# Kernel tuning notes

Measured on AMD Instinct MI355X. Metric: run time of the kernel, lower is better.

The kernel has to match this reference:

```python
import jax, jax.numpy as jnp
import numpy as np

D_MODEL = 1024
N_HEADS = 16
D_HEAD = D_MODEL // N_HEADS  # 64
NUM_MEM_KV = 4
SCALE = D_HEAD ** -0.5


def setup_inputs() -> dict:
    key = jax.random.key(0)
    k1, k2, k3, k4 = jax.random.split(key, 4)
    x = jax.random.normal(k1, (4, 4096, D_MODEL), dtype=jnp.float32)
    mask = jax.random.randint(k2, (4, 4096), 0, 2).astype(jnp.int32)
    w_qkv = jax.random.normal(k3, (3 * D_MODEL, D_MODEL), dtype=jnp.float32) * 0.02
    mem_kv = jax.random.normal(k4, (2, N_HEADS, NUM_MEM_KV, D_HEAD), dtype=jnp.float32)
    return {"x": x, "w_qkv": w_qkv, "mem_kv": mem_kv, "mask": mask}


def reference(x, w_qkv, mem_kv, mask):
    b, l, _ = x.shape
    # qkv projection: nn.Linear applies x @ W^T; reshape matches torch view(..., h, d_head, 3)
    qkv = jnp.einsum('bld,ed->ble', x, w_qkv).reshape(b, l, N_HEADS, D_HEAD, 3)
    qkv = jnp.moveaxis(qkv, 2, 1)  # (b, h, l, d_head, 3)
    q, k, v = qkv[..., 0], qkv[..., 1], qkv[..., 2]

    m = mask.astype(x.dtype)[:, None, :, None]  # (b, 1, l, 1) per prepare_mask
    k = jnp.where(m == 0, -jnp.inf, k * m)

    # prepend learned memory kv along the sequence axis
    mk = jnp.broadcast_to(mem_kv[0], (b, N_HEADS, NUM_MEM_KV, D_HEAD))
    mv = jnp.broadcast_to(mem_kv[1], (b, N_HEADS, NUM_MEM_KV, D_HEAD))
    k = jnp.concatenate([mk, k], axis=-2)  # (b, h, m+l, d_head)
    v = jnp.concatenate([mv, v], axis=-2)

    q = jax.nn.softmax(q * SCALE, axis=-1)   # softmax over feature dim
    k = jax.nn.softmax(k, axis=-2)           # softmax over sequence dim; -inf rows -> 0 weight

    context = jnp.einsum('bhnd,bhne->bhde', k, v)   # (b, h, d_head, d_head)
    out = jnp.einsum('bhld,bhde->bhle', q, context)  # (b, h, l, d_head)
    out = out * m
    out = jnp.moveaxis(out, 1, 2).reshape(b, l, N_HEADS * D_HEAD)
    return out
```

## Files before the change

kernel.cpp:

```cpp
#include <hip/hip_runtime.h>

typedef _Float16 h8 __attribute__((ext_vector_type(8)));
typedef _Float16 h4 __attribute__((ext_vector_type(4)));
typedef float f4 __attribute__((ext_vector_type(4)));

typedef __attribute__((address_space(1))) const void GV;
typedef __attribute__((address_space(3))) void SV;

__device__ __forceinline__ void async16(const void* g, void* s) {
  __builtin_amdgcn_global_load_lds((GV*)g, (SV*)s, 16, 0, 0);
}


#define XC 2097152
#define WC 393216
#define ZC 4194304

__global__ __launch_bounds__(1024) void compact(const int4* __restrict__ mask4,
                                                int* __restrict__ cnt,
                                                int* __restrict__ idx) {
  const int b = blockIdx.x;
  const int t = threadIdx.x;
  const int lane = t & 63, w = t >> 6;

  const int4 m4 = mask4[b * 1024 + t];
  int m[4] = {m4.x, m4.y, m4.z, m4.w};
  const int c = (m[0] != 0) + (m[1] != 0) + (m[2] != 0) + (m[3] != 0);

  int inc = c;
#pragma unroll
  for (int off = 1; off < 64; off <<= 1) {
    const int v = __shfl_up(inc, off);
    if (lane >= off) inc += v;
  }
  __shared__ int wtot[16];
  if (lane == 63) wtot[w] = inc;
  __syncthreads();
  int prev = 0;
#pragma unroll
  for (int i = 0; i < 16; ++i)
    if (i < w) prev += wtot[i];
  const int excl = prev + inc - c;

  if (t == 1023) cnt[b] = excl + c;

  int* const ib = idx + b * 4096;
  int p = excl;
  int q = t * 4 - excl;
#pragma unroll
  for (int r = 0; r < 4; ++r) {
    const int row = t * 4 + r;
    if (m[r]) ib[p++] = row;
    else      ib[4095 - q++] = row;
  }
}

__global__ __launch_bounds__(256) void cvt_f16(const float4* __restrict__ x,
                                               const float4* __restrict__ w,
                                               const int* __restrict__ mask,
                                               h8* __restrict__ xh,
                                               h8* __restrict__ wh,
                                               float4* __restrict__ out) {
  int t = blockIdx.x * 256 + threadIdx.x;
  if (t < XC) {
    const int row = t >> 7, c7 = t & 127;
    const int dst = (row << 7) | (c7 & 120) | ((c7 & 7) ^ (row & 7));
    float4 a = x[t * 2], b = x[t * 2 + 1];
    h8 o = {(_Float16)a.x, (_Float16)a.y, (_Float16)a.z, (_Float16)a.w,
            (_Float16)b.x, (_Float16)b.y, (_Float16)b.z, (_Float16)b.w};
    xh[dst] = o;
  } else if (t < XC + WC) {
    const int u = t - XC;
    const int rp = u >> 7, c7 = u & 127;
    int sr;
    if (rp < 2048) {
      int h = rp >> 7, c = rp & 127;
      sr = h * 192 + ((c < 64) ? (c * 3 + 1) : ((c - 64) * 3 + 2));
    } else {
      int q = rp - 2048;
      sr = (q >> 6) * 192 + (q & 63) * 3;
    }
    const int dst = (rp << 7) | (c7 & 120) | ((c7 & 7) ^ (rp & 7));
    float4 a = w[sr * 256 + c7 * 2], b = w[sr * 256 + c7 * 2 + 1];
    h8 o = {(_Float16)a.x, (_Float16)a.y, (_Float16)a.z, (_Float16)a.w,
            (_Float16)b.x, (_Float16)b.y, (_Float16)b.z, (_Float16)b.w};
    wh[dst] = o;
  } else {
    const int u = t - (XC + WC);
    const int row = u >> 8, c = u & 255;
    if (!mask[row]) {
      const float4 z4 = {0.f, 0.f, 0.f, 0.f};
      out[(size_t)row * 256 + c] = z4;
    }
  }
}

__global__ __launch_bounds__(256, 3) void kv_gemm(const _Float16* __restrict__ A,
                                                  const _Float16* __restrict__ W,
                                                  const int* __restrict__ cnt,
                                                  const int* __restrict__ idx,
                                                  float* __restrict__ part) {
  const int my = blockIdx.y;
  const int b = my >> 5, lc = my & 31;
  const int cb = cnt[b];
  if (lc * 128 >= cb) return;

  __shared__ _Float16 smem[128 * 128];
  _Float16* const As = smem;
  _Float16* const Bs = smem + 8192;
  const int tid = threadIdx.x;
  const int lane = tid & 63, wid = tid >> 6;
  const int wm = wid & 1, wn = wid >> 1;
  const int l15 = lane & 15, quad = lane >> 4;
  const int n0 = blockIdx.x * 128;

  int rsrc[4], x7[4];
#pragma unroll
  for (int it = 0; it < 4; ++it) {
    const int s = it * 32 + (tid >> 3);
    const int ri = idx[b * 4096 + lc * 128 + s];
    rsrc[it] = b * 4096 + ri;
    x7[it] = (s & 7) ^ (ri & 7);
  }
  const int cg = tid & 7;

  const f4 z = {0.f, 0.f, 0.f, 0.f};
  f4 acc[4][4];
#pragma unroll
  for (int i = 0; i < 4; ++i)
#pragma unroll
    for (int j = 0; j < 4; ++j) acc[i][j] = z;

  const int swz = l15 & 7;

  for (int kt = 0; kt < 16; ++kt) {
    const int k0 = kt * 64;
#pragma unroll
    for (int it = 0; it < 4; ++it) {
      const int idxl = it * 256 + tid;
      const int brow = idxl >> 3;
      async16(A + ((size_t)rsrc[it] * 1024 + k0 + (cg ^ x7[it]) * 8), As + idxl * 8);
      async16(W + ((size_t)(n0 + brow) * 1024 + k0 + cg * 8), Bs + idxl * 8);
    }
    __syncthreads();
#pragma unroll
    for (int ks = 0; ks < 2; ++ks) {
      const int pc = ((ks << 2) | quad) ^ swz;
      h8 af[4], bf[4];
#pragma unroll
      for (int i = 0; i < 4; ++i)
        af[i] = *(const h8*)&As[(wm * 64 + i * 16 + l15) * 64 + pc * 8];
#pragma unroll
      for (int j = 0; j < 4; ++j)
        bf[j] = *(const h8*)&Bs[(wn * 64 + j * 16 + l15) * 64 + pc * 8];
#pragma unroll
      for (int i = 0; i < 4; ++i)
#pragma unroll
        for (int j = 0; j < 4; ++j)
          acc[i][j] = __builtin_amdgcn_mfma_f32_16x16x32_f16(af[i], bf[j], acc[i][j], 0, 0, 0);
    }
    __syncthreads();
  }

  const int h = n0 >> 7;
  const int bh = b * 16 + h;
  const int jbase = lc * 128;
#pragma unroll
  for (int i = 0; i < 4; ++i) {
    const int nb = wm * 64 + i * 16 + quad * 4;
#pragma unroll
    for (int j = 0; j < 4; ++j) {
      const int c = wn * 64 + j * 16 + l15;
      h4 o;
      if (wn == 0) {
#pragma unroll
        for (int r = 0; r < 4; ++r)
          o[r] = (_Float16)((jbase + nb + r < cb) ? __expf(acc[i][j][r]) : 0.f);
      } else {
#pragma unroll
        for (int r = 0; r < 4; ++r) o[r] = (_Float16)acc[i][j][r];
      }
      *(h4*)&smem[c * 128 + (nb ^ (l15 * 8))] = o;
    }
  }
  __syncthreads();
  f4 cacc[5];
#pragma unroll
  for (int i = 0; i < 5; ++i) cacc[i] = z;
  h8 bones;
  {
    const _Float16 o1 = (l15 == 0) ? (_Float16)1.f : (_Float16)0.f;
#pragma unroll
    for (int j = 0; j < 8; ++j) bones[j] = o1;
  }
  const int ds = wid * 16;
#pragma unroll
  for (int ks = 0; ks < 4; ++ks) {
    const int nb2 = (ks * 32 + quad * 8) ^ (l15 * 8);
    h8 a = *(const h8*)&smem[(ds + l15) * 128 + nb2];
#pragma unroll
    for (int et = 0; et < 4; ++et) {
      h8 bv = *(const h8*)&smem[(64 + et * 16 + l15) * 128 + nb2];
      cacc[et] = __builtin_amdgcn_mfma_f32_16x16x32_f16(a, bv, cacc[et], 0, 0, 0);
    }
    cacc[4] = __builtin_amdgcn_mfma_f32_16x16x32_f16(a, bones, cacc[4], 0, 0, 0);
  }
  const size_t pb = ((size_t)bh * 32 + lc) * 4160;
  const int dw = ds + quad * 4;
#pragma unroll
  for (int et = 0; et < 4; ++et)
#pragma unroll
    for (int r = 0; r < 4; ++r)
      part[pb + (size_t)(dw + r) * 64 + et * 16 + l15] = cacc[et][r];
  if (l15 == 0) {
#pragma unroll
    for (int r = 0; r < 4; ++r) part[pb + 4096 + dw + r] = cacc[4][r];
  }
}

__global__ __launch_bounds__(256) void reduce_ctx(const float* __restrict__ part,
                                                  const float* __restrict__ memkv,
                                                  const int* __restrict__ cnt,
                                                  _Float16* __restrict__ ctxt) {
  const int bh = blockIdx.x;
  const int dsl = blockIdx.y;
  const int h = bh & 15;
  const int tid = threadIdx.x;
  const int dl = tid >> 6, e = tid & 63;
  const int d = dsl * 4 + dl;
  const size_t pb = (size_t)bh * 32 * 4160;
  const int nch = (cnt[bh >> 4] + 127) >> 7;

  float den = 0.f;
  for (int c = 0; c < nch; ++c) den += part[pb + (size_t)c * 4160 + 4096 + d];
  float s = 0.f;
  for (int c = 0; c < nch; ++c) s += part[pb + (size_t)c * 4160 + (size_t)d * 64 + e];
#pragma unroll
  for (int j = 0; j < 4; ++j) {
    const float ek = __expf(memkv[(h * 4 + j) * 64 + d]);
    den += ek;
    s += ek * memkv[4096 + (h * 4 + j) * 64 + e];
  }
  ctxt[(size_t)bh * 4096 + (size_t)e * 64 + d] = (_Float16)(s / den);
}

__global__ __launch_bounds__(256, 3) void qpv(const _Float16* __restrict__ A,
                                              const _Float16* __restrict__ W,
                                              const _Float16* __restrict__ ctxt,
                                              const int* __restrict__ cnt,
                                              const int* __restrict__ idx,
                                              float* __restrict__ out) {
  const int my = blockIdx.y;
  const int b = my >> 5, lc = my & 31;
  const int cb = cnt[b];
  if (lc * 128 >= cb) return;

  __shared__ _Float16 smem[128 * 128];
  _Float16* const As = smem;
  _Float16* const Bs = smem + 8192;
  const int tid = threadIdx.x;
  const int lane = tid & 63, wid = tid >> 6;
  const int wm = wid & 1, wn = wid >> 1;
  const int l15 = lane & 15, quad = lane >> 4;
  const int n0 = blockIdx.x * 128;

  int rsrc[4], x7[4];
#pragma unroll
  for (int it = 0; it < 4; ++it) {
    const int s = it * 32 + (tid >> 3);
    const int ri = idx[b * 4096 + lc * 128 + s];
    rsrc[it] = b * 4096 + ri;
    x7[it] = (s & 7) ^ (ri & 7);
  }
  const int cg = tid & 7;

  const f4 z = {0.f, 0.f, 0.f, 0.f};
  f4 acc[4][4];
#pragma unroll
  for (int i = 0; i < 4; ++i)
#pragma unroll
    for (int j = 0; j < 4; ++j) acc[i][j] = z;

  const int swz = l15 & 7;

  for (int kt = 0; kt < 16; ++kt) {
    const int k0 = kt * 64;
#pragma unroll
    for (int it = 0; it < 4; ++it) {
      const int idxl = it * 256 + tid;
      const int brow = idxl >> 3;
      async16(A + ((size_t)rsrc[it] * 1024 + k0 + (cg ^ x7[it]) * 8), As + idxl * 8);
      async16(W + ((size_t)(2048 + n0 + brow) * 1024 + k0 + cg * 8), Bs + idxl * 8);
    }
    __syncthreads();
#pragma unroll
    for (int ks = 0; ks < 2; ++ks) {
      const int pc = ((ks << 2) | quad) ^ swz;
      h8 af[4], bf[4];
#pragma unroll
      for (int i = 0; i < 4; ++i)
        af[i] = *(const h8*)&As[(wm * 64 + i * 16 + l15) * 64 + pc * 8];
#pragma unroll
      for (int j = 0; j < 4; ++j)
        bf[j] = *(const h8*)&Bs[(wn * 64 + j * 16 + l15) * 64 + pc * 8];
#pragma unroll
      for (int i = 0; i < 4; ++i)
#pragma unroll
        for (int j = 0; j < 4; ++j)
          acc[i][j] = __builtin_amdgcn_mfma_f32_16x16x32_f16(bf[j], af[i], acc[i][j], 0, 0, 0);
    }
    __syncthreads();
  }

#pragma unroll
  for (int i = 0; i < 4; ++i) {
    const int m = wm * 64 + i * 16 + l15;
    _Float16* const prow = &smem[m * 128 + wn * 64];
#pragma unroll
    for (int j = 0; j < 4; ++j) {
      h4 o;
#pragma unroll
      for (int r = 0; r < 4; ++r) o[r] = (_Float16)__expf(acc[i][j][r] * 0.125f);
      const int c3 = (j * 2 + (quad >> 1)) ^ (l15 & 7);
      *(h4*)&prow[c3 * 8 + (quad & 1) * 4] = o;
    }
  }
  __syncthreads();

  const int hw = wid >> 1;
  const int mb = (wid & 1) * 64;
  const int h = (n0 >> 6) + hw;
  const int bh = b * 16 + h;
  f4 cacc[4][5];
#pragma unroll
  for (int i = 0; i < 4; ++i)
#pragma unroll
    for (int j = 0; j < 5; ++j) cacc[i][j] = z;
  h8 bones;
  {
    const _Float16 o1 = (l15 == 0) ? (_Float16)1.f : (_Float16)0.f;
#pragma unroll
    for (int j = 0; j < 8; ++j) bones[j] = o1;
  }
#pragma unroll
  for (int ks = 0; ks < 2; ++ks) {
    h8 bf[4];
#pragma unroll
    for (int et = 0; et < 4; ++et)
      bf[et] = *(const h8*)&ctxt[(size_t)bh * 4096 +
                                 (size_t)(et * 16 + l15) * 64 + ks * 32 + quad * 8];
#pragma unroll
    for (int i2 = 0; i2 < 4; ++i2) {
      const int m = mb + i2 * 16 + l15;
      const int ch = ((ks * 4 + quad) ^ (l15 & 7)) * 8;
      h8 a = *(const h8*)&smem[m * 128 + hw * 64 + ch];
#pragma unroll
      for (int et = 0; et < 4; ++et)
        cacc[i2][et] = __builtin_amdgcn_mfma_f32_16x16x32_f16(a, bf[et], cacc[i2][et], 0, 0, 0);
      cacc[i2][4] = __builtin_amdgcn_mfma_f32_16x16x32_f16(a, bones, cacc[i2][4], 0, 0, 0);
    }
  }
#pragma unroll
  for (int i2 = 0; i2 < 4; ++i2) {
#pragma unroll
    for (int r = 0; r < 4; ++r) {
      const int s = mb + i2 * 16 + quad * 4 + r;
      const int j = lc * 128 + s;
      const float sb = __shfl(cacc[i2][4][r], lane & 48);
      if (j < cb) {
        const int row = b * 4096 + idx[b * 4096 + j];
        const float iv = 1.0f / sb;
#pragma unroll
        for (int et = 0; et < 4; ++et)
          out[(size_t)row * 1024 + h * 64 + et * 16 + l15] = cacc[i2][et][r] * iv;
      }
    }
  }
}

extern "C" void kernel_launch(void* const* d_in, const int* in_sizes, int n_in,
                              void* d_out, int out_size, void* d_ws, size_t ws_size,
                              hipStream_t stream) {
  const float* x = (const float*)d_in[0];
  const float* w = (const float*)d_in[1];
  const float* memkv = (const float*)d_in[2];
  const int* mask = (const int*)d_in[3];
  float* out = (float*)d_out;

  char* ws = (char*)d_ws;
  _Float16* xh   = (_Float16*)(ws + 0);
  _Float16* wh   = (_Float16*)(ws + 33554432);
  float*    part = (float*)(ws + 39845888);
  _Float16* ctxt = (_Float16*)(ws + 73924608);
  int*      cnt  = (int*)(ws + 74448896);
  int*      idx  = (int*)(ws + 74448928);

  compact<<<dim3(4), dim3(1024), 0, stream>>>((const int4*)mask, cnt, idx);
  cvt_f16<<<dim3(26112), dim3(256), 0, stream>>>((const float4*)x, (const float4*)w,
                                                 mask, (h8*)xh, (h8*)wh, (float4*)out);
  kv_gemm<<<dim3(16, 128), dim3(256), 0, stream>>>(xh, wh, cnt, idx, part);
  reduce_ctx<<<dim3(64, 16), dim3(256), 0, stream>>>(part, memkv, cnt, ctxt);
  qpv<<<dim3(8, 128), dim3(256), 0, stream>>>(xh, wh, ctxt, cnt, idx, out);
}
```

Measured before the change: 236.5 us.

## Pre-compact masked rows during f16 conversion so GEMMs read contiguous A

The f16 conversion kernel now gathers only the unmasked rows, in compacted order via idx, into a dense zero-padded xh buffer. It skips converting masked rows entirely. Both GEMMs then load A tiles contiguously instead of gathering rows through idx, which drops per-row index loads and scattered reads. kv_gemm's launch-bounds occupancy hint rises from 3 to 5 blocks. The conversion kernel gains per-thread cnt and idx reads.

```diff
diff --git a/kernel.cpp b/kernel.cpp
--- a/kernel.cpp
+++ b/kernel.cpp
@@ -58,17 +58,32 @@
 __global__ __launch_bounds__(256) void cvt_f16(const float4* __restrict__ x,
                                                const float4* __restrict__ w,
                                                const int* __restrict__ mask,
+                                               const int* __restrict__ cnt,
+                                               const int* __restrict__ idx,
                                                h8* __restrict__ xh,
                                                h8* __restrict__ wh,
                                                float4* __restrict__ out) {
   int t = blockIdx.x * 256 + threadIdx.x;
   if (t < XC) {
-    const int row = t >> 7, c7 = t & 127;
-    const int dst = (row << 7) | (c7 & 120) | ((c7 & 7) ^ (row & 7));
-    float4 a = x[t * 2], b = x[t * 2 + 1];
-    h8 o = {(_Float16)a.x, (_Float16)a.y, (_Float16)a.z, (_Float16)a.w,
-            (_Float16)b.x, (_Float16)b.y, (_Float16)b.z, (_Float16)b.w};
-    xh[dst] = o;
+    const int slot = t >> 7, cd = t & 127;
+    const int b = slot >> 12, s = slot & 4095;
+    const int cb = cnt[b];
+    const int lim = (cb + 127) & ~127;
+    if (s < lim) {
+      h8 o;
+      if (s < cb) {
+        const int ri = idx[b * 4096 + s];
+        const int cs = (cd & 120) | ((cd & 7) ^ (s & 7));
+        const size_t rb = (size_t)(b * 4096 + ri) * 256;
+        float4 a = x[rb + cs * 2], bb = x[rb + cs * 2 + 1];
+        o = h8{(_Float16)a.x,  (_Float16)a.y,  (_Float16)a.z,  (_Float16)a.w,
+               (_Float16)bb.x, (_Float16)bb.y, (_Float16)bb.z, (_Float16)bb.w};
+      } else {
+        o = h8{(_Float16)0.f, (_Float16)0.f, (_Float16)0.f, (_Float16)0.f,
+               (_Float16)0.f, (_Float16)0.f, (_Float16)0.f, (_Float16)0.f};
+      }
+      xh[(size_t)slot * 128 + cd] = o;
+    }
   } else if (t < XC + WC) {
     const int u = t - XC;
     const int rp = u >> 7, c7 = u & 127;
@@ -95,10 +110,9 @@
   }
 }
 
-__global__ __launch_bounds__(256, 3) void kv_gemm(const _Float16* __restrict__ A,
+__global__ __launch_bounds__(256, 5) void kv_gemm(const _Float16* __restrict__ A,
                                                   const _Float16* __restrict__ W,
                                                   const int* __restrict__ cnt,
-                                                  const int* __restrict__ idx,
                                                   float* __restrict__ part) {
   const int my = blockIdx.y;
   const int b = my >> 5, lc = my & 31;
@@ -113,16 +127,7 @@
   const int wm = wid & 1, wn = wid >> 1;
   const int l15 = lane & 15, quad = lane >> 4;
   const int n0 = blockIdx.x * 128;
-
-  int rsrc[4], x7[4];
-#pragma unroll
-  for (int it = 0; it < 4; ++it) {
-    const int s = it * 32 + (tid >> 3);
-    const int ri = idx[b * 4096 + lc * 128 + s];
-    rsrc[it] = b * 4096 + ri;
-    x7[it] = (s & 7) ^ (ri & 7);
-  }
-  const int cg = tid & 7;
+  const int m0 = b * 4096 + lc * 128;
 
   const f4 z = {0.f, 0.f, 0.f, 0.f};
   f4 acc[4][4];
@@ -138,9 +143,9 @@
 #pragma unroll
     for (int it = 0; it < 4; ++it) {
       const int idxl = it * 256 + tid;
-      const int brow = idxl >> 3;
-      async16(A + ((size_t)rsrc[it] * 1024 + k0 + (cg ^ x7[it]) * 8), As + idxl * 8);
-      async16(W + ((size_t)(n0 + brow) * 1024 + k0 + cg * 8), Bs + idxl * 8);
+      const int row = idxl >> 3, cg = idxl & 7;
+      async16(A + ((size_t)(m0 + row) * 1024 + k0 + cg * 8), As + idxl * 8);
+      async16(W + ((size_t)(n0 + row) * 1024 + k0 + cg * 8), Bs + idxl * 8);
     }
     __syncthreads();
 #pragma unroll
@@ -263,16 +268,7 @@
   const int wm = wid & 1, wn = wid >> 1;
   const int l15 = lane & 15, quad = lane >> 4;
   const int n0 = blockIdx.x * 128;
-
-  int rsrc[4], x7[4];
-#pragma unroll
-  for (int it = 0; it < 4; ++it) {
-    const int s = it * 32 + (tid >> 3);
-    const int ri = idx[b * 4096 + lc * 128 + s];
-    rsrc[it] = b * 4096 + ri;
-    x7[it] = (s & 7) ^ (ri & 7);
-  }
-  const int cg = tid & 7;
+  const int m0 = b * 4096 + lc * 128;
 
   const f4 z = {0.f, 0.f, 0.f, 0.f};
   f4 acc[4][4];
@@ -288,9 +284,9 @@
 #pragma unroll
     for (int it = 0; it < 4; ++it) {
       const int idxl = it * 256 + tid;
-      const int brow = idxl >> 3;
-      async16(A + ((size_t)rsrc[it] * 1024 + k0 + (cg ^ x7[it]) * 8), As + idxl * 8);
-      async16(W + ((size_t)(2048 + n0 + brow) * 1024 + k0 + cg * 8), Bs + idxl * 8);
+      const int row = idxl >> 3, cg = idxl & 7;
+      async16(A + ((size_t)(m0 + row) * 1024 + k0 + cg * 8), As + idxl * 8);
+      async16(W + ((size_t)(2048 + n0 + row) * 1024 + k0 + cg * 8), Bs + idxl * 8);
     }
     __syncthreads();
 #pragma unroll
@@ -397,8 +393,9 @@
 
   compact<<<dim3(4), dim3(1024), 0, stream>>>((const int4*)mask, cnt, idx);
   cvt_f16<<<dim3(26112), dim3(256), 0, stream>>>((const float4*)x, (const float4*)w,
-                                                 mask, (h8*)xh, (h8*)wh, (float4*)out);
-  kv_gemm<<<dim3(16, 128), dim3(256), 0, stream>>>(xh, wh, cnt, idx, part);
+                                                 mask, cnt, idx,
+                                                 (h8*)xh, (h8*)wh, (float4*)out);
+  kv_gemm<<<dim3(16, 128), dim3(256), 0, stream>>>(xh, wh, cnt, part);
   reduce_ctx<<<dim3(64, 16), dim3(256), 0, stream>>>(part, memkv, cnt, ctxt);
   qpv<<<dim3(8, 128), dim3(256), 0, stream>>>(xh, wh, ctxt, cnt, idx, out);
 }
```

New measurement: 274.8 us. +16.2%, slower.
